# Kernel tuning notes

Measured on AMD Instinct MI355X. Metric: run time of the kernel, lower is better.

Reference implementation:

```python
import jax, jax.numpy as jnp
import numpy as np

T = 2048        # Tmax encoder frames
EPROJS = 1024   # encoder projection dim (Henc)
DUNITS = 512    # prediction net hidden
EMBED = 512     # embedding dim
JOINT = 512     # joint space dim
ODIM = 10000    # output vocab
BLANK = 0


def setup_inputs() -> dict:
    key = jax.random.key(0)
    ks = jax.random.split(key, 11)
    def g(k, shape, scale):
        return (jax.random.normal(k, shape, dtype=jnp.float32) * scale)
    inp = {
        'h': jax.random.normal(ks[0], (T, EPROJS), dtype=jnp.float32),
        # Embedding with padding_idx=blank -> blank row zeroed
        'embed': g(ks[1], (ODIM, EMBED), 0.05).at[BLANK].set(0.0),
        # LSTMCell params (torch gate order: i, f, g, o)
        'W_ih': g(ks[2], (4 * DUNITS, EMBED), 1.0 / np.sqrt(EMBED)),
        'W_hh': g(ks[3], (4 * DUNITS, DUNITS), 1.0 / np.sqrt(DUNITS)),
        'b_ih': g(ks[4], (4 * DUNITS,), 0.01),
        'b_hh': g(ks[5], (4 * DUNITS,), 0.01),
        # joint network
        'W_enc': g(ks[6], (JOINT, EPROJS), 1.0 / np.sqrt(EPROJS)),
        'b_enc': g(ks[7], (JOINT,), 0.01),
        'W_dec': g(ks[8], (JOINT, DUNITS), 1.0 / np.sqrt(DUNITS)),  # no bias
        'W_out': g(ks[9], (ODIM, JOINT), 1.0 / np.sqrt(JOINT)),
        'b_out': g(ks[10], (ODIM,), 0.01),
    }
    return inp


def _lstm_cell(x, h_prev, c_prev, W_ih, W_hh, b_ih, b_hh):
    gates = W_ih @ x + b_ih + W_hh @ h_prev + b_hh  # (4*DUNITS,)
    i, f, g, o = jnp.split(gates, 4)
    c = jax.nn.sigmoid(f) * c_prev + jax.nn.sigmoid(i) * jnp.tanh(g)
    h = jax.nn.sigmoid(o) * jnp.tanh(c)
    return h, c


def reference(h, embed, W_ih, W_hh, b_ih, b_hh, W_enc, b_enc, W_dec, W_out, b_out):
    # Precompute encoder-side joint projection (same math, hoisted out of loop)
    h_proj = h @ W_enc.T + b_enc  # (T, JOINT)

    # Initial prediction-net step on zero embedding from zero state
    zeros_e = jnp.zeros((EMBED,), dtype=h.dtype)
    zeros_d = jnp.zeros((DUNITS,), dtype=h.dtype)
    y0, c0 = _lstm_cell(zeros_e, zeros_d, zeros_d, W_ih, W_hh, b_ih, b_hh)

    def step(carry, hp_t):
        y, c, score = carry
        # joint: tanh(lin_enc(h_t) + lin_dec(y)) -> lin_out -> log_softmax
        ytu = jax.nn.log_softmax(W_out @ jnp.tanh(hp_t + W_dec @ y) + b_out)
        logp = jnp.max(ytu)
        pred = jnp.argmax(ytu)
        emitted = pred != BLANK
        # Candidate prediction-net update with embedded token
        ey = embed[pred]
        y_new, c_new = _lstm_cell(ey, y, c, W_ih, W_hh, b_ih, b_hh)
        y = jnp.where(emitted, y_new, y)
        c = jnp.where(emitted, c_new, c)
        score = score + jnp.where(emitted, logp, jnp.zeros_like(logp))
        tok = jnp.where(emitted, pred, BLANK).astype(jnp.int32)
        return (y, c, score), tok

    (y, c, score), yseq = jax.lax.scan(step, (y0, c0, jnp.float32(0.0)), h_proj)
    # yseq: (T,) int32, BLANK where no symbol was emitted at that frame
    return yseq, score
```

## Files before the change

### kernel.cpp

```cpp
#include <hip/hip_runtime.h>
#include <stdint.h>

typedef unsigned long long u64;
typedef uint32_t u32;

#define NB     256
#define NT     256
#define TMAX   2048
#define EPROJS 1024
#define DUNITS 512
#define EMBED  512
#define JOINT  512
#define ODIM   10000

#define N_LSTM 32
#define DEC0   32
#define CONS0  48
#define N_CONS 208
#define MAGIC  0xD07ED07Eu

#define WS_YB   0
#define WS_UD   4096
#define WS_PK   8192
#define WS_SA   10240
#define WS_DN   12288
#define WS_HP   16384

__device__ __forceinline__ float aloadf(const float* p){
  return __hip_atomic_load(p, __ATOMIC_RELAXED, __HIP_MEMORY_SCOPE_AGENT);
}
__device__ __forceinline__ void astoref(float* p, float v){
  __hip_atomic_store(p, v, __ATOMIC_RELAXED, __HIP_MEMORY_SCOPE_AGENT);
}
__device__ __forceinline__ u64 aloadu64(const u64* p){
  return __hip_atomic_load(p, __ATOMIC_RELAXED, __HIP_MEMORY_SCOPE_AGENT);
}
__device__ __forceinline__ void astoreu64(u64* p, u64 v){
  __hip_atomic_store(p, v, __ATOMIC_RELAXED, __HIP_MEMORY_SCOPE_AGENT);
}
__device__ __forceinline__ u32 aloadu32(const u32* p){
  return __hip_atomic_load(p, __ATOMIC_RELAXED, __HIP_MEMORY_SCOPE_AGENT);
}
__device__ __forceinline__ void astoreu32(u32* p, u32 v){
  __hip_atomic_store(p, v, __ATOMIC_RELAXED, __HIP_MEMORY_SCOPE_AGENT);
}

__device__ __forceinline__ u32 ordbits(float f){
  u32 u = __float_as_uint(f);
  return (u & 0x80000000u) ? ~u : (u | 0x80000000u);
}
__device__ __forceinline__ float unordbits(u32 o){
  u32 u = (o & 0x80000000u) ? (o & 0x7fffffffu) : ~o;
  return __uint_as_float(u);
}
__device__ __forceinline__ float sigmoidf_(float x){ return 1.0f/(1.0f+expf(-x)); }

__device__ __forceinline__ float wredsum(float v){
  #pragma unroll
  for (int o=32;o>0;o>>=1) v += __shfl_xor(v, o);
  return v;
}
__device__ __forceinline__ u64 wredmax64(u64 v){
  #pragma unroll
  for (int o=32;o>0;o>>=1){ u64 x = __shfl_xor(v, o); v = (x>v)?x:v; }
  return v;
}

#define LOAD8(dst, baseptr) { const float4* _p=(const float4*)(baseptr); \
  float4 _a=_p[0], _b=_p[1]; \
  dst[0]=_a.x; dst[1]=_a.y; dst[2]=_a.z; dst[3]=_a.w; \
  dst[4]=_b.x; dst[5]=_b.y; dst[6]=_b.z; dst[7]=_b.w; }

#define LDS8(dst, base) { float4 _a=*(const float4*)(base); \
  float4 _b=*(const float4*)((base)+4); \
  dst[0]=_a.x; dst[1]=_a.y; dst[2]=_a.z; dst[3]=_a.w; \
  dst[4]=_b.x; dst[5]=_b.y; dst[6]=_b.z; dst[7]=_b.w; }

__global__ void rnnt_init(char* ws){
  u32* p = (u32*)ws;
  for (int i = threadIdx.x; i < 4096; i += blockDim.x) p[i] = 0u;
}

__global__ void __launch_bounds__(NT, 1)
rnnt_decode(const float* __restrict__ h,    const float* __restrict__ embed,
            const float* __restrict__ W_ih, const float* __restrict__ W_hh,
            const float* __restrict__ b_ih, const float* __restrict__ b_hh,
            const float* __restrict__ W_enc,const float* __restrict__ b_enc,
            const float* __restrict__ W_dec,const float* __restrict__ W_out,
            const float* __restrict__ b_out,
            float* __restrict__ out, char* __restrict__ ws)
{
  const int b    = blockIdx.x;
  const int tid  = threadIdx.x;
  const int lane = tid & 63;
  const int w    = tid >> 6;

  u64*   ybuf = (u64*)(ws + WS_YB);
  u64*   udec = (u64*)(ws + WS_UD);
  u64*   packs= (u64*)(ws + WS_PK);
  u64*   sarr = (u64*)(ws + WS_SA);
  u32*   done = (u32*)(ws + WS_DN);
  float* hp   = (float*)(ws + WS_HP);

  __shared__ float smem[8192];
  float* PL = smem;
  float* EL = &smem[4416];
  float* YL = &smem[4928];
  float* ZL = &smem[5440];
  float* GL = &smem[5952];
  u64*   R64= (u64*)&smem[6016];
  float* RF = &smem[6024];

  {
    float (*lds_h)[EPROJS] = (float(*)[EPROJS])smem;
    #pragma unroll
    for (int r=0;r<8;r++){
      const float4 hv = *(const float4*)(h + (size_t)(8*b + r)*EPROJS + tid*4);
      *(float4*)&lds_h[r][tid*4] = hv;
    }
    __syncthreads();
    for (int p=0;p<2;p++){
      const int j = p*NT + tid;
      float acc[8] = {0,0,0,0,0,0,0,0};
      const float4* wrow = (const float4*)(W_enc + (size_t)j*EPROJS);
      for (int k4=0;k4<EPROJS/4;k4++){
        const float4 wv = wrow[k4];
        #pragma unroll
        for (int t8=0;t8<8;t8++){
          const float4 hv = *(const float4*)&lds_h[t8][k4*4];
          acc[t8] = fmaf(wv.x,hv.x, fmaf(wv.y,hv.y, fmaf(wv.z,hv.z, fmaf(wv.w,hv.w, acc[t8]))));
        }
      }
      const float be = b_enc[j];
      #pragma unroll
      for (int t8=0;t8<8;t8++)
        astoref(&hp[(size_t)(8*b+t8)*JOINT + j], acc[t8] + be);
    }
    asm volatile("s_waitcnt vmcnt(0)" ::: "memory");
    if (tid==0) astoreu32(&done[b], MAGIC);
    __syncthreads();
  }

  if (b < N_LSTM){
    const int d = b;
    float wih[16][8], whh[16][8];
    #pragma unroll
    for (int q=0;q<16;q++){
      const int gr = w*DUNITS + 16*d + q;
      LOAD8(wih[q], W_ih + (size_t)gr*EMBED  + lane*8);
      LOAD8(whh[q], W_hh + (size_t)gr*DUNITS + lane*8);
    }
    float bias_r = 0.0f;
    if (tid < 64){
      const int gr = (tid>>4)*DUNITS + 16*d + (tid&15);
      bias_r = b_ih[gr] + b_hh[gr];
    }
    float c_st = 0.0f, y_st = 0.0f;
    if (tid < 16){
      const int j = 16*d + tid;
      const float gi = b_ih[j]            + b_hh[j];
      const float gg = b_ih[2*DUNITS + j] + b_hh[2*DUNITS + j];
      const float go = b_ih[3*DUNITS + j] + b_hh[3*DUNITS + j];
      c_st = sigmoidf_(gi)*tanhf(gg);
      y_st = sigmoidf_(go)*tanhf(c_st);
      astoreu64(&ybuf[j], ((u64)1u<<32) | (u64)__float_as_uint(y_st));
    }

    for (int t=0;t<TMAX;t++){
      const u32 tg = (u32)(t+1);
      u64 ya, yb;
      for(;;){
        ya = aloadu64(&ybuf[2*tid]); yb = aloadu64(&ybuf[2*tid+1]);
        const int ok = ((u32)(ya>>32)==tg) & ((u32)(yb>>32)==tg);
        if (__syncthreads_and(ok)) break;
      }
      YL[2*tid]   = __uint_as_float((u32)ya);
      YL[2*tid+1] = __uint_as_float((u32)yb);
      __syncthreads();
      float y8[8]; LDS8(y8, &YL[8*lane]);
      float vp[16];
      #pragma unroll
      for (int q=0;q<16;q++){
        float a=0.f;
        #pragma unroll
        for (int k=0;k<8;k++) a = fmaf(whh[q][k], y8[k], a);
        vp[q] = a;
      }
      u64 pk = 0;
      for(;;){
        if (tid < N_CONS) pk = aloadu64(&packs[tid]);
        const int ok = (tid < N_CONS) ? ((u32)(pk>>48)==tg) : 1;
        if (__syncthreads_and(ok)) break;
      }
      { u64 m = wredmax64(pk); if (lane==0) R64[w]=m; }
      __syncthreads();
      if (tid==0){
        u64 bb=R64[0];
        #pragma unroll
        for (int i=1;i<4;i++) bb = (R64[i]>bb)?R64[i]:bb;
        R64[0]=bb;
      }
      __syncthreads();
      const u64 best = R64[0];
      const int pred = (int)((~(u32)best) & 0xFFFFu);
      const int emitted = (pred != 0);
      __syncthreads();
      const float2 ev = *(const float2*)(embed + (size_t)pred*EMBED + 2*tid);
      EL[2*tid] = ev.x; EL[2*tid+1] = ev.y;
      __syncthreads();
      float e8[8]; LDS8(e8, &EL[8*lane]);
      #pragma unroll
      for (int q=0;q<16;q++){
        float a = vp[q];
        #pragma unroll
        for (int k=0;k<8;k++) a = fmaf(wih[q][k], e8[k], a);
        PL[(w*16+q)*68 + lane] = a;
      }
      __syncthreads();
      if (tid < 64){
        const float* row = &PL[tid*68];
        float s = bias_r;
        #pragma unroll
        for (int k4=0;k4<16;k4++){
          const float4 v4 = *(const float4*)&row[4*k4];
          s += v4.x + v4.y + v4.z + v4.w;
        }
        GL[tid] = s;
      }
      __syncthreads();
      if (tid < 16){
        const float gi=GL[tid], gf=GL[16+tid], gg=GL[32+tid], go=GL[48+tid];
        const float cn = sigmoidf_(gf)*c_st + sigmoidf_(gi)*tanhf(gg);
        const float yn = sigmoidf_(go)*tanhf(cn);
        if (emitted){ c_st = cn; y_st = yn; }
        astoreu64(&ybuf[16*d + tid], ((u64)(tg+1)<<32) | (u64)__float_as_uint(y_st));
      }
    }
  }
  else if (b < CONS0){
    const int dd = b - DEC0;
    float wdec[8][8];
    #pragma unroll
    for (int q=0;q<8;q++){
      const int r = 32*dd + 8*w + q;
      LOAD8(wdec[q], W_dec + (size_t)r*DUNITS + lane*8);
    }
    for (int t=0;t<TMAX;t++){
      const u32 tg = (u32)(t+1);
      u64 ya, yb;
      for(;;){
        ya = aloadu64(&ybuf[2*tid]); yb = aloadu64(&ybuf[2*tid+1]);
        const int ok = ((u32)(ya>>32)==tg) & ((u32)(yb>>32)==tg);
        if (__syncthreads_and(ok)) break;
      }
      YL[2*tid]   = __uint_as_float((u32)ya);
      YL[2*tid+1] = __uint_as_float((u32)yb);
      __syncthreads();
      float y8[8]; LDS8(y8, &YL[8*lane]);
      #pragma unroll
      for (int q=0;q<8;q++){
        float a=0.f;
        #pragma unroll
        for (int k=0;k<8;k++) a = fmaf(wdec[q][k], y8[k], a);
        PL[(8*w+q)*68 + lane] = a;
      }
      __syncthreads();
      if (tid < 32){
        const float* row = &PL[tid*68];
        float s = 0.f;
        #pragma unroll
        for (int k4=0;k4<16;k4++){
          const float4 v4 = *(const float4*)&row[4*k4];
          s += v4.x + v4.y + v4.z + v4.w;
        }
        astoreu64(&udec[32*dd + tid], ((u64)tg<<32) | (u64)__float_as_uint(s));
      }
      __syncthreads();
    }
  }
  else {
    const int cb = b - CONS0;
    const int rowstart = (cb<16) ? cb*49 : 784 + (cb-16)*48;
    const int rowcnt   = (cb<16) ? 49 : 48;
    float wout[13][8];
    #pragma unroll
    for (int q=0;q<13;q++){
      const int s = 13*w + q;
      if (s < rowcnt){
        LOAD8(wout[q], W_out + (size_t)(rowstart+s)*JOINT + lane*8);
      } else {
        #pragma unroll
        for (int k=0;k<8;k++) wout[q][k]=0.f;
      }
    }
    float my_bo = 0.f; int my_row = 0; bool my_val = false;
    if (tid < rowcnt){ my_val = true; my_row = rowstart + tid; my_bo = b_out[my_row]; }

    for(;;){
      const int ok = (aloadu32(&done[tid]) == MAGIC);
      if (__syncthreads_and(ok)) break;
    }

    float score = 0.0f;
    for (int t=0;t<TMAX;t++){
      const u32 tg = (u32)(t+1);
      u64 ua, ub;
      for(;;){
        ua = aloadu64(&udec[2*tid]); ub = aloadu64(&udec[2*tid+1]);
        const int ok = ((u32)(ua>>32)==tg) & ((u32)(ub>>32)==tg);
        if (__syncthreads_and(ok)) break;
      }
      const float u0 = __uint_as_float((u32)ua);
      const float u1 = __uint_as_float((u32)ub);
      const float h0 = aloadf(&hp[(size_t)t*JOINT + 2*tid]);
      const float h1 = aloadf(&hp[(size_t)t*JOINT + 2*tid + 1]);
      ZL[2*tid]   = tanhf(h0 + u0);
      ZL[2*tid+1] = tanhf(h1 + u1);
      __syncthreads();
      float z8[8]; LDS8(z8, &ZL[8*lane]);
      #pragma unroll
      for (int q=0;q<13;q++){
        float a=0.f;
        #pragma unroll
        for (int k=0;k<8;k++) a = fmaf(wout[q][k], z8[k], a);
        PL[(13*w+q)*68 + lane] = a;
      }
      __syncthreads();
      u64 key = 0; float lg = 0.f;
      if (tid < 52){
        const float* row = &PL[tid*68];
        float s = my_bo;
        #pragma unroll
        for (int k4=0;k4<16;k4++){
          const float4 v4 = *(const float4*)&row[4*k4];
          s += v4.x + v4.y + v4.z + v4.w;
        }
        lg = s;
        if (my_val) key = ((u64)ordbits(lg)<<16) | (u64)(0xFFFFu & ~(u32)my_row);
      }
      if (w == 0){
        const u64 bk = wredmax64(key);
        const float mw = unordbits((u32)(bk>>16));
        const float e  = my_val ? __expf(lg - mw) : 0.f;
        const float sw = wredsum(e);
        if (lane == 0){
          astoreu64(&sarr[cb],  ((u64)tg<<32) | (u64)__float_as_uint(sw));
          astoreu64(&packs[cb], ((u64)tg<<48) | bk);
        }
      }
      if (b == CONS0){
        u64 pk = 0, sa = 0;
        for(;;){
          if (tid < N_CONS){ pk = aloadu64(&packs[tid]); sa = aloadu64(&sarr[tid]); }
          const int ok = (tid < N_CONS) ?
            (((u32)(pk>>48)==tg) & ((u32)(sa>>32)==tg)) : 1;
          if (__syncthreads_and(ok)) break;
        }
        { u64 m = wredmax64(pk); if (lane==0) R64[w]=m; }
        __syncthreads();
        if (tid==0){
          u64 bb=R64[0];
          #pragma unroll
          for (int i=1;i<4;i++) bb = (R64[i]>bb)?R64[i]:bb;
          R64[0]=bb;
        }
        __syncthreads();
        const u64 best = R64[0];
        const float mstar = unordbits((u32)(best>>16));
        float term = (tid < N_CONS) ?
          __uint_as_float((u32)sa) * __expf(unordbits((u32)(pk>>16)) - mstar) : 0.f;
        term = wredsum(term);
        if (lane==0) RF[w]=term;
        __syncthreads();
        if (tid==0){
          const float S = RF[0]+RF[1]+RF[2]+RF[3];
          const int pred = (int)((~(u32)best) & 0xFFFFu);
          if (pred != 0) score += -logf(S);
          out[t] = (float)pred;
        }
        __syncthreads();
      } else {
        __syncthreads();
      }
    }
    if (b == CONS0 && tid == 0) out[TMAX] = score;
  }
}

extern "C" void kernel_launch(void* const* d_in, const int* in_sizes, int n_in,
                              void* d_out, int out_size, void* d_ws, size_t ws_size,
                              hipStream_t stream)
{
  const float* h     = (const float*)d_in[0];
  const float* embed = (const float*)d_in[1];
  const float* W_ih  = (const float*)d_in[2];
  const float* W_hh  = (const float*)d_in[3];
  const float* b_ih  = (const float*)d_in[4];
  const float* b_hh  = (const float*)d_in[5];
  const float* W_enc = (const float*)d_in[6];
  const float* b_enc = (const float*)d_in[7];
  const float* W_dec = (const float*)d_in[8];
  const float* W_out = (const float*)d_in[9];
  const float* b_out = (const float*)d_in[10];
  float* out = (float*)d_out;
  char* ws = (char*)d_ws;

  hipLaunchKernelGGL(rnnt_init, dim3(1), dim3(NT), 0, stream, ws);
  hipLaunchKernelGGL(rnnt_decode, dim3(NB), dim3(NT), 0, stream,
                     h, embed, W_ih, W_hh, b_ih, b_hh, W_enc, b_enc, W_dec, W_out, b_out,
                     out, ws);
}
```

Measured before the change: 18.70 ms.

## Restructure persistent decode pipeline with ring-buffered packs, dedicated scorer and warp-level polling

Shrinks the persistent grid from 256 to 174 blocks, with encoder-projection work strided across blocks. The decoder blocks now compute tanh(hp+W_dec y) directly and publish z, so output blocks skip that step. Each output block handles 80 rows per step and reduces argmax and softmax partials in registers, using warp shuffles instead of LDS partial-sum tables. A separate scorer block consumes a 4-deep ring of packs/sums so output blocks can run ahead, and polling uses __all within a warp rather than block-wide __syncthreads_and. This cuts per-step barrier and sync latency on the serial critical path, at the cost of more shuffle reductions and extra ring-progress spinning.

```diff
diff --git a/kernel.cpp b/kernel.cpp
--- a/kernel.cpp
+++ b/kernel.cpp
@@ -4,7 +4,7 @@
 typedef unsigned long long u64;
 typedef uint32_t u32;
 
-#define NB     256
+#define NBLK   174
 #define NT     256
 #define TMAX   2048
 #define EPROJS 1024
@@ -13,18 +13,24 @@
 #define JOINT  512
 #define ODIM   10000
 
-#define N_LSTM 32
-#define DEC0   32
-#define CONS0  48
-#define N_CONS 208
-#define MAGIC  0xD07ED07Eu
-
-#define WS_YB   0
-#define WS_UD   4096
-#define WS_PK   8192
-#define WS_SA   10240
-#define WS_DN   12288
-#define WS_HP   16384
+#define N_LSTM  32
+#define B_DEC0  32
+#define N_DEC   16
+#define B_SCORE 48
+#define B_CONS0 49
+#define N_CONS  125
+#define RPW     20
+#define MAGIC   0xD07ED07Eu
+#define RING    4
+#define RMASK   3
+
+#define WS_YB 0
+#define WS_ZB 4096
+#define WS_PK 8192
+#define WS_SM 12288
+#define WS_DN 16384
+#define WS_SP 17408
+#define WS_HP 32768
 
 __device__ __forceinline__ float aloadf(const float* p){
   return __hip_atomic_load(p, __ATOMIC_RELAXED, __HIP_MEMORY_SCOPE_AGENT);
@@ -66,19 +72,25 @@
   return v;
 }
 
-#define LOAD8(dst, baseptr) { const float4* _p=(const float4*)(baseptr); \
-  float4 _a=_p[0], _b=_p[1]; \
-  dst[0]=_a.x; dst[1]=_a.y; dst[2]=_a.z; dst[3]=_a.w; \
-  dst[4]=_b.x; dst[5]=_b.y; dst[6]=_b.z; dst[7]=_b.w; }
-
-#define LDS8(dst, base) { float4 _a=*(const float4*)(base); \
-  float4 _b=*(const float4*)((base)+4); \
-  dst[0]=_a.x; dst[1]=_a.y; dst[2]=_a.z; dst[3]=_a.w; \
-  dst[4]=_b.x; dst[5]=_b.y; dst[6]=_b.z; dst[7]=_b.w; }
+__device__ __forceinline__ void pollbuf8(const u64* buf, int lane, u32 tg, float* o){
+  for(;;){
+    u64 v[8];
+    #pragma unroll
+    for (int j=0;j<8;j++) v[j] = aloadu64(&buf[64*j + lane]);
+    int ok = 1;
+    #pragma unroll
+    for (int j=0;j<8;j++) ok &= ((u32)(v[j]>>32) == tg);
+    if (__all(ok)){
+      #pragma unroll
+      for (int j=0;j<8;j++) o[j] = __uint_as_float((u32)v[j]);
+      return;
+    }
+  }
+}
 
 __global__ void rnnt_init(char* ws){
   u32* p = (u32*)ws;
-  for (int i = threadIdx.x; i < 4096; i += blockDim.x) p[i] = 0u;
+  for (int i = threadIdx.x; i < 8192; i += blockDim.x) p[i] = 0u;
 }
 
 __global__ void __launch_bounds__(NT, 1)
@@ -95,46 +107,46 @@
   const int lane = tid & 63;
   const int w    = tid >> 6;
 
-  u64*   ybuf = (u64*)(ws + WS_YB);
-  u64*   udec = (u64*)(ws + WS_UD);
-  u64*   packs= (u64*)(ws + WS_PK);
-  u64*   sarr = (u64*)(ws + WS_SA);
-  u32*   done = (u32*)(ws + WS_DN);
-  float* hp   = (float*)(ws + WS_HP);
+  u64*   ybuf  = (u64*)(ws + WS_YB);
+  u64*   zbuf  = (u64*)(ws + WS_ZB);
+  u64*   packs = (u64*)(ws + WS_PK);
+  u64*   sums  = (u64*)(ws + WS_SM);
+  u32*   done  = (u32*)(ws + WS_DN);
+  u32*   sprog = (u32*)(ws + WS_SP);
+  float* hp    = (float*)(ws + WS_HP);
 
   __shared__ float smem[8192];
-  float* PL = smem;
-  float* EL = &smem[4416];
-  float* YL = &smem[4928];
-  float* ZL = &smem[5440];
-  float* GL = &smem[5952];
-  u64*   R64= (u64*)&smem[6016];
-  float* RF = &smem[6024];
+  float* ZL = smem;
+  u64*   R64= (u64*)&smem[512];
+  float* RF = &smem[520];
 
   {
     float (*lds_h)[EPROJS] = (float(*)[EPROJS])smem;
-    #pragma unroll
-    for (int r=0;r<8;r++){
-      const float4 hv = *(const float4*)(h + (size_t)(8*b + r)*EPROJS + tid*4);
-      *(float4*)&lds_h[r][tid*4] = hv;
-    }
-    __syncthreads();
-    for (int p=0;p<2;p++){
-      const int j = p*NT + tid;
-      float acc[8] = {0,0,0,0,0,0,0,0};
-      const float4* wrow = (const float4*)(W_enc + (size_t)j*EPROJS);
-      for (int k4=0;k4<EPROJS/4;k4++){
-        const float4 wv = wrow[k4];
-        #pragma unroll
-        for (int t8=0;t8<8;t8++){
-          const float4 hv = *(const float4*)&lds_h[t8][k4*4];
-          acc[t8] = fmaf(wv.x,hv.x, fmaf(wv.y,hv.y, fmaf(wv.z,hv.z, fmaf(wv.w,hv.w, acc[t8]))));
+    for (int s = b; s < 256; s += NBLK){
+      __syncthreads();
+      #pragma unroll
+      for (int r=0;r<8;r++){
+        const float4 hv = *(const float4*)(h + (size_t)(8*s + r)*EPROJS + tid*4);
+        *(float4*)&lds_h[r][tid*4] = hv;
+      }
+      __syncthreads();
+      for (int p=0;p<2;p++){
+        const int j = p*NT + tid;
+        float acc[8] = {0,0,0,0,0,0,0,0};
+        const float4* wrow = (const float4*)(W_enc + (size_t)j*EPROJS);
+        for (int k4=0;k4<EPROJS/4;k4++){
+          const float4 wv = wrow[k4];
+          #pragma unroll
+          for (int t8=0;t8<8;t8++){
+            const float4 hv = *(const float4*)&lds_h[t8][k4*4];
+            acc[t8] = fmaf(wv.x,hv.x, fmaf(wv.y,hv.y, fmaf(wv.z,hv.z, fmaf(wv.w,hv.w, acc[t8]))));
+          }
         }
-      }
-      const float be = b_enc[j];
-      #pragma unroll
-      for (int t8=0;t8<8;t8++)
-        astoref(&hp[(size_t)(8*b+t8)*JOINT + j], acc[t8] + be);
+        const float be = b_enc[j];
+        #pragma unroll
+        for (int t8=0;t8<8;t8++)
+          astoref(&hp[(size_t)(8*s+t8)*JOINT + j], acc[t8] + be);
+      }
     }
     asm volatile("s_waitcnt vmcnt(0)" ::: "memory");
     if (tid==0) astoreu32(&done[b], MAGIC);
@@ -143,247 +155,206 @@
 
   if (b < N_LSTM){
     const int d = b;
-    float wih[16][8], whh[16][8];
-    #pragma unroll
-    for (int q=0;q<16;q++){
-      const int gr = w*DUNITS + 16*d + q;
-      LOAD8(wih[q], W_ih + (size_t)gr*EMBED  + lane*8);
-      LOAD8(whh[q], W_hh + (size_t)gr*DUNITS + lane*8);
-    }
-    float bias_r = 0.0f;
-    if (tid < 64){
-      const int gr = (tid>>4)*DUNITS + 16*d + (tid&15);
-      bias_r = b_ih[gr] + b_hh[gr];
-    }
-    float c_st = 0.0f, y_st = 0.0f;
-    if (tid < 16){
-      const int j = 16*d + tid;
-      const float gi = b_ih[j]            + b_hh[j];
-      const float gg = b_ih[2*DUNITS + j] + b_hh[2*DUNITS + j];
-      const float go = b_ih[3*DUNITS + j] + b_hh[3*DUNITS + j];
-      c_st = sigmoidf_(gi)*tanhf(gg);
-      y_st = sigmoidf_(go)*tanhf(c_st);
-      astoreu64(&ybuf[j], ((u64)1u<<32) | (u64)__float_as_uint(y_st));
+    float wih[16][8], whh[16][8], bias[16];
+    #pragma unroll
+    for (int m=0;m<16;m++){
+      const int g = m>>2, j = m&3;
+      const int r = g*DUNITS + 16*d + 4*w + j;
+      #pragma unroll
+      for (int k=0;k<8;k++){
+        wih[m][k] = W_ih[(size_t)r*EMBED  + 64*k + lane];
+        whh[m][k] = W_hh[(size_t)r*DUNITS + 64*k + lane];
+      }
+      bias[m] = b_ih[r] + b_hh[r];
+    }
+    float c_st[4], y_st[4];
+    #pragma unroll
+    for (int j=0;j<4;j++){
+      c_st[j] = sigmoidf_(bias[j]) * tanhf(bias[8+j]);
+      y_st[j] = sigmoidf_(bias[12+j]) * tanhf(c_st[j]);
+    }
+    if (lane < 4){
+      float yv = y_st[0];
+      #pragma unroll
+      for (int j=1;j<4;j++) if (lane==j) yv = y_st[j];
+      astoreu64(&ybuf[16*d + 4*w + lane], ((u64)1u<<32) | (u64)__float_as_uint(yv));
     }
 
     for (int t=0;t<TMAX;t++){
       const u32 tg = (u32)(t+1);
-      u64 ya, yb;
+      float y8[8]; pollbuf8(ybuf, lane, tg, y8);
+      float gt[16];
+      #pragma unroll
+      for (int m=0;m<16;m++){
+        float a=0.f;
+        #pragma unroll
+        for (int k=0;k<8;k++) a = fmaf(whh[m][k], y8[k], a);
+        gt[m] = wredsum(a) + bias[m];
+      }
+      const u64* pk_s = packs + (t & RMASK)*128;
+      u64 p0, p1;
+      const u64 dummy = ((u64)tg << 48);
       for(;;){
-        ya = aloadu64(&ybuf[2*tid]); yb = aloadu64(&ybuf[2*tid+1]);
-        const int ok = ((u32)(ya>>32)==tg) & ((u32)(yb>>32)==tg);
-        if (__syncthreads_and(ok)) break;
-      }
-      YL[2*tid]   = __uint_as_float((u32)ya);
-      YL[2*tid+1] = __uint_as_float((u32)yb);
+        p0 = aloadu64(&pk_s[lane]);
+        p1 = (lane < N_CONS-64) ? aloadu64(&pk_s[64+lane]) : dummy;
+        const int ok = ((u32)(p0>>48)==tg) & ((u32)(p1>>48)==tg);
+        if (__all(ok)) break;
+      }
+      u64 best = (p0>p1)?p0:p1;
+      best = wredmax64(best);
+      const int pred = (int)((~(u32)best) & 0xFFFFu);
+      const int emitted = (pred != 0);
+      float e8[8];
+      #pragma unroll
+      for (int k=0;k<8;k++) e8[k] = embed[(size_t)pred*EMBED + 64*k + lane];
+      #pragma unroll
+      for (int m=0;m<16;m++){
+        float a=0.f;
+        #pragma unroll
+        for (int k=0;k<8;k++) a = fmaf(wih[m][k], e8[k], a);
+        gt[m] += wredsum(a);
+      }
+      #pragma unroll
+      for (int j=0;j<4;j++){
+        const float gi=gt[j], gf=gt[4+j], gg=gt[8+j], go=gt[12+j];
+        const float cn = sigmoidf_(gf)*c_st[j] + sigmoidf_(gi)*tanhf(gg);
+        const float yn = sigmoidf_(go)*tanhf(cn);
+        if (emitted){ c_st[j]=cn; y_st[j]=yn; }
+      }
+      if (lane < 4){
+        float yv = y_st[0];
+        #pragma unroll
+        for (int j=1;j<4;j++) if (lane==j) yv = y_st[j];
+        astoreu64(&ybuf[16*d + 4*w + lane], ((u64)(tg+1)<<32) | (u64)__float_as_uint(yv));
+      }
+    }
+  }
+  else if (b < B_DEC0 + N_DEC){
+    const int i = b - B_DEC0;
+    float wdec[8][8];
+    #pragma unroll
+    for (int q=0;q<8;q++){
+      const int r = 32*i + 8*w + q;
+      #pragma unroll
+      for (int k=0;k<8;k++) wdec[q][k] = W_dec[(size_t)r*DUNITS + 64*k + lane];
+    }
+    for(;;){
+      const u32 d0 = aloadu32(&done[lane]);
+      const u32 d1 = aloadu32(&done[64+lane]);
+      const u32 d2 = (lane < NBLK-128) ? aloadu32(&done[128+lane]) : MAGIC;
+      if (__all((d0==MAGIC) & (d1==MAGIC) & (d2==MAGIC))) break;
+    }
+    for (int t=0;t<TMAX;t++){
+      const u32 tg = (u32)(t+1);
+      const float hpv = (lane<8) ? hp[(size_t)t*JOINT + 32*i + 8*w + lane] : 0.f;
+      float y8[8]; pollbuf8(ybuf, lane, tg, y8);
+      float tot[8];
+      #pragma unroll
+      for (int q=0;q<8;q++){
+        float a=0.f;
+        #pragma unroll
+        for (int k=0;k<8;k++) a = fmaf(wdec[q][k], y8[k], a);
+        tot[q] = wredsum(a);
+      }
+      if (lane < 8){
+        float u = tot[0];
+        #pragma unroll
+        for (int q=1;q<8;q++) if (lane==q) u = tot[q];
+        const float z = tanhf(hpv + u);
+        astoreu64(&zbuf[32*i + 8*w + lane], ((u64)tg<<32) | (u64)__float_as_uint(z));
+      }
+    }
+  }
+  else if (b == B_SCORE){
+    if (w == 0){
+      float score = 0.0f;
+      for (int t=0;t<TMAX;t++){
+        const u32 tg = (u32)(t+1);
+        const u64* pk_s = packs + (t & RMASK)*128;
+        const u64* sm_s = sums  + (t & RMASK)*128;
+        u64 p0=0,p1=0,s0=0,s1=0;
+        const int v1 = (lane < N_CONS-64);
+        for(;;){
+          p0 = aloadu64(&pk_s[lane]);   s0 = aloadu64(&sm_s[lane]);
+          int ok = ((u32)(p0>>48)==tg) & ((u32)(s0>>32)==tg);
+          if (v1){
+            p1 = aloadu64(&pk_s[64+lane]); s1 = aloadu64(&sm_s[64+lane]);
+            ok &= ((u32)(p1>>48)==tg) & ((u32)(s1>>32)==tg);
+          }
+          if (__all(ok)) break;
+        }
+        u64 best = (p0>p1)?p0:p1;
+        best = wredmax64(best);
+        const float mstar = unordbits((u32)(best>>16));
+        const int pred = (int)((~(u32)best) & 0xFFFFu);
+        float term = __uint_as_float((u32)s0) * __expf(unordbits((u32)(p0>>16)) - mstar);
+        if (v1) term += __uint_as_float((u32)s1) * __expf(unordbits((u32)(p1>>16)) - mstar);
+        term = wredsum(term);
+        if (pred != 0) score += -logf(term);
+        if (lane==0){
+          out[t] = (float)pred;
+          astoreu32(sprog, tg);
+        }
+      }
+      if (lane==0) out[TMAX] = score;
+    }
+  }
+  else {
+    const int cb = b - B_CONS0;
+    const int rowstart = cb*80 + w*RPW;
+    float wout[RPW][8]; float bo[RPW];
+    #pragma unroll
+    for (int q=0;q<RPW;q++){
+      const int r = rowstart + q;
+      #pragma unroll
+      for (int k=0;k<8;k++) wout[q][k] = W_out[(size_t)r*JOINT + 64*k + lane];
+      bo[q] = b_out[r];
+    }
+    for (int t=0;t<TMAX;t++){
+      const u32 tg = (u32)(t+1);
+      if (w == 0){
+        float zs[8]; pollbuf8(zbuf, lane, tg, zs);
+        #pragma unroll
+        for (int j=0;j<8;j++) ZL[64*j + lane] = zs[j];
+      }
       __syncthreads();
-      float y8[8]; LDS8(y8, &YL[8*lane]);
-      float vp[16];
-      #pragma unroll
-      for (int q=0;q<16;q++){
+      float z8[8];
+      #pragma unroll
+      for (int j=0;j<8;j++) z8[j] = ZL[64*j + lane];
+      float lg[RPW];
+      #pragma unroll
+      for (int q=0;q<RPW;q++){
         float a=0.f;
         #pragma unroll
-        for (int k=0;k<8;k++) a = fmaf(whh[q][k], y8[k], a);
-        vp[q] = a;
-      }
-      u64 pk = 0;
-      for(;;){
-        if (tid < N_CONS) pk = aloadu64(&packs[tid]);
-        const int ok = (tid < N_CONS) ? ((u32)(pk>>48)==tg) : 1;
-        if (__syncthreads_and(ok)) break;
-      }
-      { u64 m = wredmax64(pk); if (lane==0) R64[w]=m; }
+        for (int k=0;k<8;k++) a = fmaf(wout[q][k], z8[k], a);
+        lg[q] = wredsum(a) + bo[q];
+      }
+      u64 bk = 0;
+      #pragma unroll
+      for (int q=0;q<RPW;q++){
+        const u64 key = ((u64)ordbits(lg[q])<<16) | (u64)(0xFFFFu & ~(u32)(rowstart+q));
+        bk = (key>bk)?key:bk;
+      }
+      const float mw = unordbits((u32)(bk>>16));
+      float sw = 0.f;
+      #pragma unroll
+      for (int q=0;q<RPW;q++) sw += __expf(lg[q]-mw);
+      if (lane==0){ R64[w] = bk; RF[w] = sw; }
       __syncthreads();
       if (tid==0){
-        u64 bb=R64[0];
-        #pragma unroll
-        for (int i=1;i<4;i++) bb = (R64[i]>bb)?R64[i]:bb;
-        R64[0]=bb;
-      }
-      __syncthreads();
-      const u64 best = R64[0];
-      const int pred = (int)((~(u32)best) & 0xFFFFu);
-      const int emitted = (pred != 0);
-      __syncthreads();
-      const float2 ev = *(const float2*)(embed + (size_t)pred*EMBED + 2*tid);
-      EL[2*tid] = ev.x; EL[2*tid+1] = ev.y;
-      __syncthreads();
-      float e8[8]; LDS8(e8, &EL[8*lane]);
-      #pragma unroll
-      for (int q=0;q<16;q++){
-        float a = vp[q];
-        #pragma unroll
-        for (int k=0;k<8;k++) a = fmaf(wih[q][k], e8[k], a);
-        PL[(w*16+q)*68 + lane] = a;
-      }
-      __syncthreads();
-      if (tid < 64){
-        const float* row = &PL[tid*68];
-        float s = bias_r;
-        #pragma unroll
-        for (int k4=0;k4<16;k4++){
-          const float4 v4 = *(const float4*)&row[4*k4];
-          s += v4.x + v4.y + v4.z + v4.w;
-        }
-        GL[tid] = s;
-      }
-      __syncthreads();
-      if (tid < 16){
-        const float gi=GL[tid], gf=GL[16+tid], gg=GL[32+tid], go=GL[48+tid];
-        const float cn = sigmoidf_(gf)*c_st + sigmoidf_(gi)*tanhf(gg);
-        const float yn = sigmoidf_(go)*tanhf(cn);
-        if (emitted){ c_st = cn; y_st = yn; }
-        astoreu64(&ybuf[16*d + tid], ((u64)(tg+1)<<32) | (u64)__float_as_uint(y_st));
-      }
-    }
-  }
-  else if (b < CONS0){
-    const int dd = b - DEC0;
-    float wdec[8][8];
-    #pragma unroll
-    for (int q=0;q<8;q++){
-      const int r = 32*dd + 8*w + q;
-      LOAD8(wdec[q], W_dec + (size_t)r*DUNITS + lane*8);
-    }
-    for (int t=0;t<TMAX;t++){
-      const u32 tg = (u32)(t+1);
-      u64 ya, yb;
-      for(;;){
-        ya = aloadu64(&ybuf[2*tid]); yb = aloadu64(&ybuf[2*tid+1]);
-        const int ok = ((u32)(ya>>32)==tg) & ((u32)(yb>>32)==tg);
-        if (__syncthreads_and(ok)) break;
-      }
-      YL[2*tid]   = __uint_as_float((u32)ya);
-      YL[2*tid+1] = __uint_as_float((u32)yb);
-      __syncthreads();
-      float y8[8]; LDS8(y8, &YL[8*lane]);
-      #pragma unroll
-      for (int q=0;q<8;q++){
-        float a=0.f;
-        #pragma unroll
-        for (int k=0;k<8;k++) a = fmaf(wdec[q][k], y8[k], a);
-        PL[(8*w+q)*68 + lane] = a;
-      }
-      __syncthreads();
-      if (tid < 32){
-        const float* row = &PL[tid*68];
-        float s = 0.f;
-        #pragma unroll
-        for (int k4=0;k4<16;k4++){
-          const float4 v4 = *(const float4*)&row[4*k4];
-          s += v4.x + v4.y + v4.z + v4.w;
-        }
-        astoreu64(&udec[32*dd + tid], ((u64)tg<<32) | (u64)__float_as_uint(s));
-      }
-      __syncthreads();
-    }
-  }
-  else {
-    const int cb = b - CONS0;
-    const int rowstart = (cb<16) ? cb*49 : 784 + (cb-16)*48;
-    const int rowcnt   = (cb<16) ? 49 : 48;
-    float wout[13][8];
-    #pragma unroll
-    for (int q=0;q<13;q++){
-      const int s = 13*w + q;
-      if (s < rowcnt){
-        LOAD8(wout[q], W_out + (size_t)(rowstart+s)*JOINT + lane*8);
-      } else {
-        #pragma unroll
-        for (int k=0;k<8;k++) wout[q][k]=0.f;
-      }
-    }
-    float my_bo = 0.f; int my_row = 0; bool my_val = false;
-    if (tid < rowcnt){ my_val = true; my_row = rowstart + tid; my_bo = b_out[my_row]; }
-
-    for(;;){
-      const int ok = (aloadu32(&done[tid]) == MAGIC);
-      if (__syncthreads_and(ok)) break;
-    }
-
-    float score = 0.0f;
-    for (int t=0;t<TMAX;t++){
-      const u32 tg = (u32)(t+1);
-      u64 ua, ub;
-      for(;;){
-        ua = aloadu64(&udec[2*tid]); ub = aloadu64(&udec[2*tid+1]);
-        const int ok = ((u32)(ua>>32)==tg) & ((u32)(ub>>32)==tg);
-        if (__syncthreads_and(ok)) break;
-      }
-      const float u0 = __uint_as_float((u32)ua);
-      const float u1 = __uint_as_float((u32)ub);
-      const float h0 = aloadf(&hp[(size_t)t*JOINT + 2*tid]);
-      const float h1 = aloadf(&hp[(size_t)t*JOINT + 2*tid + 1]);
-      ZL[2*tid]   = tanhf(h0 + u0);
-      ZL[2*tid+1] = tanhf(h1 + u1);
-      __syncthreads();
-      float z8[8]; LDS8(z8, &ZL[8*lane]);
-      #pragma unroll
-      for (int q=0;q<13;q++){
-        float a=0.f;
-        #pragma unroll
-        for (int k=0;k<8;k++) a = fmaf(wout[q][k], z8[k], a);
-        PL[(13*w+q)*68 + lane] = a;
-      }
-      __syncthreads();
-      u64 key = 0; float lg = 0.f;
-      if (tid < 52){
-        const float* row = &PL[tid*68];
-        float s = my_bo;
-        #pragma unroll
-        for (int k4=0;k4<16;k4++){
-          const float4 v4 = *(const float4*)&row[4*k4];
-          s += v4.x + v4.y + v4.z + v4.w;
-        }
-        lg = s;
-        if (my_val) key = ((u64)ordbits(lg)<<16) | (u64)(0xFFFFu & ~(u32)my_row);
-      }
-      if (w == 0){
-        const u64 bk = wredmax64(key);
-        const float mw = unordbits((u32)(bk>>16));
-        const float e  = my_val ? __expf(lg - mw) : 0.f;
-        const float sw = wredsum(e);
-        if (lane == 0){
-          astoreu64(&sarr[cb],  ((u64)tg<<32) | (u64)__float_as_uint(sw));
-          astoreu64(&packs[cb], ((u64)tg<<48) | bk);
-        }
-      }
-      if (b == CONS0){
-        u64 pk = 0, sa = 0;
-        for(;;){
-          if (tid < N_CONS){ pk = aloadu64(&packs[tid]); sa = aloadu64(&sarr[tid]); }
-          const int ok = (tid < N_CONS) ?
-            (((u32)(pk>>48)==tg) & ((u32)(sa>>32)==tg)) : 1;
-          if (__syncthreads_and(ok)) break;
-        }
-        { u64 m = wredmax64(pk); if (lane==0) R64[w]=m; }
-        __syncthreads();
-        if (tid==0){
-          u64 bb=R64[0];
-          #pragma unroll
-          for (int i=1;i<4;i++) bb = (R64[i]>bb)?R64[i]:bb;
-          R64[0]=bb;
-        }
-        __syncthreads();
-        const u64 best = R64[0];
-        const float mstar = unordbits((u32)(best>>16));
-        float term = (tid < N_CONS) ?
-          __uint_as_float((u32)sa) * __expf(unordbits((u32)(pk>>16)) - mstar) : 0.f;
-        term = wredsum(term);
-        if (lane==0) RF[w]=term;
-        __syncthreads();
-        if (tid==0){
-          const float S = RF[0]+RF[1]+RF[2]+RF[3];
-          const int pred = (int)((~(u32)best) & 0xFFFFu);
-          if (pred != 0) score += -logf(S);
-          out[t] = (float)pred;
-        }
-        __syncthreads();
-      } else {
-        __syncthreads();
-      }
-    }
-    if (b == CONS0 && tid == 0) out[TMAX] = score;
+        u64 bb = R64[0];
+        #pragma unroll
+        for (int k=1;k<4;k++) bb = (R64[k]>bb)?R64[k]:bb;
+        const float mb = unordbits((u32)(bb>>16));
+        float S = 0.f;
+        #pragma unroll
+        for (int k=0;k<4;k++) S += RF[k]*__expf(unordbits((u32)(R64[k]>>16)) - mb);
+        while ((int)aloadu32(sprog) < t-3){ __builtin_amdgcn_s_sleep(1); }
+        const int slot = t & RMASK;
+        astoreu64(&sums [slot*128 + cb], ((u64)tg<<32) | (u64)__float_as_uint(S));
+        astoreu64(&packs[slot*128 + cb], ((u64)tg<<48) | bb);
+      }
+    }
   }
 }
 
@@ -406,7 +377,7 @@
   char* ws = (char*)d_ws;
 
   hipLaunchKernelGGL(rnnt_init, dim3(1), dim3(NT), 0, stream, ws);
-  hipLaunchKernelGGL(rnnt_decode, dim3(NB), dim3(NT), 0, stream,
+  hipLaunchKernelGGL(rnnt_decode, dim3(NBLK), dim3(NT), 0, stream,
                      h, embed, W_ih, W_hh, b_ih, b_hh, W_enc, b_enc, W_dec, W_out, b_out,
                      out, ws);
 }
```

After: 24.84 ms. 1.33x slower.
